# Kernel optimization log

Hardware: AMD Instinct MI355X
Metric: run time of the kernel (lower is better)

Reference implementation:

```python
import jax, jax.numpy as jnp
import numpy as np

N_NODES, N_EDGES = 50000, 200000
DN, DE, DG = 256, 256, 128

def setup_inputs() -> dict:
    key = jax.random.key(0)
    ks = jax.random.split(key, 8)
    s = lambda d: 1.0 / np.sqrt(d)
    return {
        "nodes": jax.random.normal(ks[0], (N_NODES, DN), jnp.float32),
        "edges": jax.random.normal(ks[1], (N_EDGES, DE), jnp.float32),
        "globals_": jax.random.normal(ks[2], (DG,), jnp.float32),
        "senders": jax.random.randint(ks[3], (N_EDGES,), 0, N_NODES, jnp.int32),
        "receivers": jax.random.randint(ks[4], (N_EDGES,), 0, N_NODES, jnp.int32),
        "We": jax.random.normal(ks[5], (DE + 2 * DN + DG, DE), jnp.float32) * s(DE + 2 * DN + DG),
        "be": jnp.zeros((DE,), jnp.float32),
        "Wn": jax.random.normal(ks[6], (DE + DN + DG, DN), jnp.float32) * s(DE + DN + DG),
        "bn": jnp.zeros((DN,), jnp.float32),
        "Wg": jax.random.normal(ks[7], (DE + DN + DG, DG), jnp.float32) * s(DE + DN + DG),
        "bg": jnp.zeros((DG,), jnp.float32),
    }

def reference(nodes, edges, globals_, senders, receivers, We, be, Wn, bn, Wg, bg):
    E, N = edges.shape[0], nodes.shape[0]
    # --- edge processor: phi_e([e, v_s, v_r, u]) ---
    edge_in = jnp.concatenate(
        [edges, nodes[senders], nodes[receivers],
         jnp.broadcast_to(globals_, (E, globals_.shape[0]))], axis=-1)  # [E, 896]
    new_edges = jax.nn.relu(edge_in @ We + be)  # [E, DE]
    # --- node processor: phi_v([sum_incoming_e, v, u]) ---
    agg_e = jax.ops.segment_sum(new_edges, receivers, num_segments=N)  # [N, DE]
    node_in = jnp.concatenate(
        [agg_e, nodes, jnp.broadcast_to(globals_, (N, globals_.shape[0]))], axis=-1)
    new_nodes = jax.nn.relu(node_in @ Wn + bn)  # [N, DN]
    # --- global processor: phi_u([sum_e, sum_v, u]) ---
    global_in = jnp.concatenate(
        [new_edges.sum(axis=0), new_nodes.sum(axis=0), globals_], axis=-1)
    new_globals = jax.nn.relu(global_in @ Wg + bg)  # [DG]
    return new_edges, new_nodes, new_globals
```

## Files before the change

kernel.cpp:

```cpp
#include <hip/hip_runtime.h>

#define E_CNT 200000
#define N_CNT 50000

typedef __attribute__((ext_vector_type(8))) unsigned short ushort8;
typedef __attribute__((ext_vector_type(4))) float f32x4;
typedef __bf16 bf16x8 __attribute__((ext_vector_type(8)));

static __device__ __forceinline__ unsigned short f2bf(float f) {
  unsigned int u = __builtin_bit_cast(unsigned int, f);
  u += 0x7FFFu + ((u >> 16) & 1u);
  return (unsigned short)(u >> 16);
}

__global__ void prep_w(const float* __restrict__ W, unsigned short* __restrict__ Bp, int KC) {
  int idx = blockIdx.x * blockDim.x + threadIdx.x;
  int total = KC * 16 * 64;
  if (idx >= total) return;
  int lane = idx & 63;
  int t = idx >> 6;
  int F = t & 15;
  int kc = t >> 4;
  int col = F * 16 + (lane & 15);
  int kb = kc * 32 + (lane >> 4) * 8;
  ushort8 v;
#pragma unroll
  for (int j = 0; j < 8; ++j) v[j] = f2bf(W[(size_t)(kb + j) * 256 + col]);
  *reinterpret_cast<ushort8*>(Bp + (size_t)idx * 8) = v;
}

template <int NSTEPS, bool EDGE>
__global__ __launch_bounds__(512) void gemm_mlp(
    const float* __restrict__ in0, const float* __restrict__ nodes,
    const float* __restrict__ gl, const int* __restrict__ senders,
    const int* __restrict__ receivers, const unsigned short* __restrict__ Bp,
    const float* __restrict__ bias, float* __restrict__ out,
    float* __restrict__ agg, int M) {
  __shared__ unsigned short lds[128 * 64];

  const int tid = threadIdx.x;
  const int lane = tid & 63;
  const int wave = tid >> 6;
  const int wm = wave >> 2;
  const int wn = wave & 3;
  const int row0 = blockIdx.x * 128;

  const int sr = tid >> 2;
  const int sc = tid & 3;
  int er = row0 + sr;
  if (er > M - 1) er = M - 1;

  const float* bases[4];
  if (EDGE) {
    int si = senders[er], ri = receivers[er];
    bases[0] = in0 + (size_t)er * 256;
    bases[1] = nodes + (size_t)si * 256;
    bases[2] = nodes + (size_t)ri * 256;
    bases[3] = gl;
  } else {
    bases[0] = in0 + (size_t)er * 256;
    bases[1] = nodes + (size_t)er * 256;
    bases[2] = gl;
    bases[3] = gl;
  }

  const int swz = sr & 7;
  const int wbase = sr * 64;

  f32x4 acc[4][4] = {};

#pragma unroll
  for (int ks = 0; ks < NSTEPS; ++ks) {
    const float* srcp = bases[ks >> 2] + (ks & 3) * 64 + sc * 16;
    const float4* p4 = reinterpret_cast<const float4*>(srcp);
    float fv[16];
    *reinterpret_cast<float4*>(&fv[0]) = p4[0];
    *reinterpret_cast<float4*>(&fv[4]) = p4[1];
    *reinterpret_cast<float4*>(&fv[8]) = p4[2];
    *reinterpret_cast<float4*>(&fv[12]) = p4[3];
    ushort8 w0, w1;
#pragma unroll
    for (int j = 0; j < 8; ++j) {
      w0[j] = f2bf(fv[j]);
      w1[j] = f2bf(fv[8 + j]);
    }
    int s0 = (sc * 2) ^ swz;
    int s1 = (sc * 2 + 1) ^ swz;
    *reinterpret_cast<ushort8*>(&lds[wbase + s0 * 8]) = w0;
    *reinterpret_cast<ushort8*>(&lds[wbase + s1 * 8]) = w1;
    __syncthreads();

#pragma unroll
    for (int kk = 0; kk < 2; ++kk) {
      bf16x8 a[4];
#pragma unroll
      for (int fm = 0; fm < 4; ++fm) {
        int r = wm * 64 + fm * 16 + (lane & 15);
        int slot = (kk * 4 + (lane >> 4)) ^ (r & 7);
        a[fm] = __builtin_bit_cast(
            bf16x8, *reinterpret_cast<const ushort8*>(&lds[r * 64 + slot * 8]));
      }
      bf16x8 b[4];
      const int kc32 = ks * 2 + kk;
#pragma unroll
      for (int fn = 0; fn < 4; ++fn) {
        int F = wn * 4 + fn;
        b[fn] = __builtin_bit_cast(
            bf16x8, *reinterpret_cast<const ushort8*>(
                        Bp + ((size_t)(kc32 * 16 + F) * 64 + lane) * 8));
      }
#pragma unroll
      for (int fm = 0; fm < 4; ++fm)
#pragma unroll
        for (int fn = 0; fn < 4; ++fn)
          acc[fm][fn] = __builtin_amdgcn_mfma_f32_16x16x32_bf16(
              a[fm], b[fn], acc[fm][fn], 0, 0, 0);
    }
    __syncthreads();
  }

  float bcol[4];
#pragma unroll
  for (int fn = 0; fn < 4; ++fn) bcol[fn] = bias[(wn * 4 + fn) * 16 + (lane & 15)];
#pragma unroll
  for (int fm = 0; fm < 4; ++fm) {
    int rb = row0 + wm * 64 + fm * 16 + ((lane >> 4) << 2);
#pragma unroll
    for (int i = 0; i < 4; ++i) {
      int gr = rb + i;
      if (gr < M) {
        int rcv = 0;
        if (EDGE) rcv = receivers[gr];
#pragma unroll
        for (int fn = 0; fn < 4; ++fn) {
          int col = (wn * 4 + fn) * 16 + (lane & 15);
          float v = fmaxf(acc[fm][fn][i] + bcol[fn], 0.0f);
          out[(size_t)gr * 256 + col] = v;
          if (EDGE) atomicAdd(agg + (size_t)rcv * 256 + col, v);
        }
      }
    }
  }
}

__global__ void colsum(const float* __restrict__ in, float* __restrict__ out, int rows) {
  int c = threadIdx.x;
  float s = 0.f;
  for (int r = blockIdx.x; r < rows; r += gridDim.x) s += in[(size_t)r * 256 + c];
  atomicAdd(out + c, s);
}

__global__ void global_mlp(const float* __restrict__ esum, const float* __restrict__ nsum,
                           const float* __restrict__ gl, const float* __restrict__ Wg,
                           const float* __restrict__ bg, float* __restrict__ out2) {
  int g = threadIdx.x;
  float acc = bg[g];
  for (int k = 0; k < 256; ++k) acc += esum[k] * Wg[(size_t)k * 128 + g];
  for (int k = 0; k < 256; ++k) acc += nsum[k] * Wg[(size_t)(256 + k) * 128 + g];
  for (int k = 0; k < 128; ++k) acc += gl[k] * Wg[(size_t)(512 + k) * 128 + g];
  out2[g] = fmaxf(acc, 0.f);
}

extern "C" void kernel_launch(void* const* d_in, const int* in_sizes, int n_in,
                              void* d_out, int out_size, void* d_ws, size_t ws_size,
                              hipStream_t stream) {
  const float* nodes = (const float*)d_in[0];
  const float* edges = (const float*)d_in[1];
  const float* gl = (const float*)d_in[2];
  const int* senders = (const int*)d_in[3];
  const int* receivers = (const int*)d_in[4];
  const float* We = (const float*)d_in[5];
  const float* be = (const float*)d_in[6];
  const float* Wn = (const float*)d_in[7];
  const float* bn = (const float*)d_in[8];
  const float* Wg = (const float*)d_in[9];
  const float* bg = (const float*)d_in[10];

  float* out0 = (float*)d_out;
  float* out1 = out0 + (size_t)E_CNT * 256;
  float* out2 = out1 + (size_t)N_CNT * 256;

  char* ws = (char*)d_ws;
  float* agg = (float*)ws;
  float* esum = (float*)(ws + 51200000);
  float* nsum = (float*)(ws + 51201024);
  unsigned short* BpE = (unsigned short*)(ws + 51202048);
  unsigned short* BpN = (unsigned short*)(ws + 51660800);

  hipMemsetAsync(agg, 0, 51202048, stream);

  prep_w<<<112, 256, 0, stream>>>(We, BpE, 28);
  prep_w<<<80, 256, 0, stream>>>(Wn, BpN, 20);

  gemm_mlp<14, true><<<(E_CNT + 127) / 128, 512, 0, stream>>>(
      edges, nodes, gl, senders, receivers, BpE, be, out0, agg, E_CNT);

  colsum<<<256, 256, 0, stream>>>(agg, esum, N_CNT);

  gemm_mlp<10, false><<<(N_CNT + 127) / 128, 512, 0, stream>>>(
      agg, nodes, gl, nullptr, nullptr, BpN, bn, out1, nullptr, N_CNT);

  colsum<<<256, 256, 0, stream>>>(out1, nsum, N_CNT);

  global_mlp<<<1, 128, 0, stream>>>(esum, nsum, gl, Wg, bg, out2);
}
```

Before: 471.1 us.

## Double-buffer LDS in GEMM, prefetch next K-step, vectorize colsum, parallelize global MLP

The GEMM kernel now double-buffers the A tile in LDS. It prefetches the next K-step's global loads into registers while MFMAs run on the current buffer, which halves the barriers per step. B fragments for both sub-steps are loaded up front, launch bounds request 2 blocks per CU, and edge outputs use nontemporal stores. colsum switches to float4 loads with 64-thread blocks, and global_mlp splits the K reduction across 512 threads. The changes trade higher register and LDS use for better latency hiding, and the occupancy hint may cause register spills.

```diff
diff --git a/kernel.cpp b/kernel.cpp
--- a/kernel.cpp
+++ b/kernel.cpp
@@ -30,13 +30,13 @@
 }
 
 template <int NSTEPS, bool EDGE>
-__global__ __launch_bounds__(512) void gemm_mlp(
+__global__ __launch_bounds__(512, 2) void gemm_mlp(
     const float* __restrict__ in0, const float* __restrict__ nodes,
     const float* __restrict__ gl, const int* __restrict__ senders,
     const int* __restrict__ receivers, const unsigned short* __restrict__ Bp,
     const float* __restrict__ bias, float* __restrict__ out,
     float* __restrict__ agg, int M) {
-  __shared__ unsigned short lds[128 * 64];
+  __shared__ unsigned short lds[2][128 * 64];
 
   const int tid = threadIdx.x;
   const int lane = tid & 63;
@@ -66,13 +66,13 @@
 
   const int swz = sr & 7;
   const int wbase = sr * 64;
+  const int s0 = ((sc * 2) ^ swz) * 8;
+  const int s1 = ((sc * 2 + 1) ^ swz) * 8;
 
   f32x4 acc[4][4] = {};
 
-#pragma unroll
-  for (int ks = 0; ks < NSTEPS; ++ks) {
-    const float* srcp = bases[ks >> 2] + (ks & 3) * 64 + sc * 16;
-    const float4* p4 = reinterpret_cast<const float4*>(srcp);
+  {
+    const float4* p4 = reinterpret_cast<const float4*>(bases[0] + sc * 16);
     float fv[16];
     *reinterpret_cast<float4*>(&fv[0]) = p4[0];
     *reinterpret_cast<float4*>(&fv[4]) = p4[1];
@@ -84,11 +84,37 @@
       w0[j] = f2bf(fv[j]);
       w1[j] = f2bf(fv[8 + j]);
     }
-    int s0 = (sc * 2) ^ swz;
-    int s1 = (sc * 2 + 1) ^ swz;
-    *reinterpret_cast<ushort8*>(&lds[wbase + s0 * 8]) = w0;
-    *reinterpret_cast<ushort8*>(&lds[wbase + s1 * 8]) = w1;
-    __syncthreads();
+    *reinterpret_cast<ushort8*>(&lds[0][wbase + s0]) = w0;
+    *reinterpret_cast<ushort8*>(&lds[0][wbase + s1]) = w1;
+  }
+  __syncthreads();
+
+#pragma unroll
+  for (int ks = 0; ks < NSTEPS; ++ks) {
+    const int cc = ks & 1;
+
+    bf16x8 bfr[2][4];
+#pragma unroll
+    for (int kk = 0; kk < 2; ++kk) {
+      const int kc32 = ks * 2 + kk;
+#pragma unroll
+      for (int fn = 0; fn < 4; ++fn) {
+        const int F = wn * 4 + fn;
+        bfr[kk][fn] = __builtin_bit_cast(
+            bf16x8, *reinterpret_cast<const ushort8*>(
+                        Bp + ((size_t)(kc32 * 16 + F) * 64 + lane) * 8));
+      }
+    }
+
+    float4 nf0, nf1, nf2, nf3;
+    if (ks + 1 < NSTEPS) {
+      const float4* p4 = reinterpret_cast<const float4*>(
+          bases[(ks + 1) >> 2] + ((ks + 1) & 3) * 64 + sc * 16);
+      nf0 = p4[0];
+      nf1 = p4[1];
+      nf2 = p4[2];
+      nf3 = p4[3];
+    }
 
 #pragma unroll
     for (int kk = 0; kk < 2; ++kk) {
@@ -98,25 +124,32 @@
         int r = wm * 64 + fm * 16 + (lane & 15);
         int slot = (kk * 4 + (lane >> 4)) ^ (r & 7);
         a[fm] = __builtin_bit_cast(
-            bf16x8, *reinterpret_cast<const ushort8*>(&lds[r * 64 + slot * 8]));
-      }
-      bf16x8 b[4];
-      const int kc32 = ks * 2 + kk;
-#pragma unroll
-      for (int fn = 0; fn < 4; ++fn) {
-        int F = wn * 4 + fn;
-        b[fn] = __builtin_bit_cast(
-            bf16x8, *reinterpret_cast<const ushort8*>(
-                        Bp + ((size_t)(kc32 * 16 + F) * 64 + lane) * 8));
+            bf16x8, *reinterpret_cast<const ushort8*>(&lds[cc][r * 64 + slot * 8]));
       }
 #pragma unroll
       for (int fm = 0; fm < 4; ++fm)
 #pragma unroll
         for (int fn = 0; fn < 4; ++fn)
           acc[fm][fn] = __builtin_amdgcn_mfma_f32_16x16x32_bf16(
-              a[fm], b[fn], acc[fm][fn], 0, 0, 0);
-    }
-    __syncthreads();
+              a[fm], bfr[kk][fn], acc[fm][fn], 0, 0, 0);
+    }
+
+    if (ks + 1 < NSTEPS) {
+      float fv[16];
+      *reinterpret_cast<float4*>(&fv[0]) = nf0;
+      *reinterpret_cast<float4*>(&fv[4]) = nf1;
+      *reinterpret_cast<float4*>(&fv[8]) = nf2;
+      *reinterpret_cast<float4*>(&fv[12]) = nf3;
+      ushort8 w0, w1;
+#pragma unroll
+      for (int j = 0; j < 8; ++j) {
+        w0[j] = f2bf(fv[j]);
+        w1[j] = f2bf(fv[8 + j]);
+      }
+      *reinterpret_cast<ushort8*>(&lds[cc ^ 1][wbase + s0]) = w0;
+      *reinterpret_cast<ushort8*>(&lds[cc ^ 1][wbase + s1]) = w1;
+      __syncthreads();
+    }
   }
 
   float bcol[4];
@@ -135,8 +168,12 @@
         for (int fn = 0; fn < 4; ++fn) {
           int col = (wn * 4 + fn) * 16 + (lane & 15);
           float v = fmaxf(acc[fm][fn][i] + bcol[fn], 0.0f);
-          out[(size_t)gr * 256 + col] = v;
-          if (EDGE) atomicAdd(agg + (size_t)rcv * 256 + col, v);
+          if (EDGE) {
+            __builtin_nontemporal_store(v, &out[(size_t)gr * 256 + col]);
+            atomicAdd(agg + (size_t)rcv * 256 + col, v);
+          } else {
+            out[(size_t)gr * 256 + col] = v;
+          }
         }
       }
     }
@@ -144,21 +181,33 @@
 }
 
 __global__ void colsum(const float* __restrict__ in, float* __restrict__ out, int rows) {
-  int c = threadIdx.x;
-  float s = 0.f;
-  for (int r = blockIdx.x; r < rows; r += gridDim.x) s += in[(size_t)r * 256 + c];
-  atomicAdd(out + c, s);
+  int c4 = threadIdx.x;
+  f32x4 s = {0.f, 0.f, 0.f, 0.f};
+  for (int r = blockIdx.x; r < rows; r += gridDim.x) {
+    f32x4 v = *reinterpret_cast<const f32x4*>(in + (size_t)r * 256 + c4 * 4);
+    s += v;
+  }
+#pragma unroll
+  for (int j = 0; j < 4; ++j) atomicAdd(out + c4 * 4 + j, s[j]);
 }
 
 __global__ void global_mlp(const float* __restrict__ esum, const float* __restrict__ nsum,
                            const float* __restrict__ gl, const float* __restrict__ Wg,
                            const float* __restrict__ bg, float* __restrict__ out2) {
-  int g = threadIdx.x;
-  float acc = bg[g];
-  for (int k = 0; k < 256; ++k) acc += esum[k] * Wg[(size_t)k * 128 + g];
-  for (int k = 0; k < 256; ++k) acc += nsum[k] * Wg[(size_t)(256 + k) * 128 + g];
-  for (int k = 0; k < 128; ++k) acc += gl[k] * Wg[(size_t)(512 + k) * 128 + g];
-  out2[g] = fmaxf(acc, 0.f);
+  __shared__ float red[512];
+  int g = threadIdx.x & 127;
+  int kg = threadIdx.x >> 7;
+  float acc = 0.f;
+  for (int k = kg; k < 640; k += 4) {
+    float x = (k < 256) ? esum[k] : (k < 512 ? nsum[k - 256] : gl[k - 512]);
+    acc += x * Wg[(size_t)k * 128 + g];
+  }
+  red[threadIdx.x] = acc;
+  __syncthreads();
+  if (kg == 0) {
+    float r = red[g] + red[128 + g] + red[256 + g] + red[384 + g] + bg[g];
+    out2[g] = fmaxf(r, 0.f);
+  }
 }
 
 extern "C" void kernel_launch(void* const* d_in, const int* in_sizes, int n_in,
@@ -195,12 +244,12 @@
   gemm_mlp<14, true><<<(E_CNT + 127) / 128, 512, 0, stream>>>(
       edges, nodes, gl, senders, receivers, BpE, be, out0, agg, E_CNT);
 
-  colsum<<<256, 256, 0, stream>>>(agg, esum, N_CNT);
+  colsum<<<512, 64, 0, stream>>>(agg, esum, N_CNT);
 
   gemm_mlp<10, false><<<(N_CNT + 127) / 128, 512, 0, stream>>>(
       agg, nodes, gl, nullptr, nullptr, BpN, bn, out1, nullptr, N_CNT);
 
-  colsum<<<256, 256, 0, stream>>>(out1, nsum, N_CNT);
-
-  global_mlp<<<1, 128, 0, stream>>>(esum, nsum, gl, Wg, bg, out2);
-}
+  colsum<<<512, 64, 0, stream>>>(out1, nsum, N_CNT);
+
+  global_mlp<<<1, 512, 0, stream>>>(esum, nsum, gl, Wg, bg, out2);
+}
```

Result: slower. 568.0 us (+20.6%).
